# Performance work log

Hardware: AMD Instinct MI355X
Metric: run time of the kernel (lower is better)

## Reference

```python
import jax, jax.numpy as jnp
import numpy as np


def setup_inputs() -> dict:
    key = jax.random.key(0)
    z = jax.random.normal(key, (8, 4096, 1024), dtype=jnp.float32)
    return {"z": z}


def reference(z):
    d = z.shape[-1]
    # sort descending along last dim
    z_sorted = -jnp.sort(-z, axis=-1)
    z_cumsum = jnp.cumsum(z_sorted, axis=-1)
    k = jnp.arange(1, d + 1, dtype=z.dtype)  # [d]
    rhs = 1 + k * z_sorted
    is_gt = (rhs > z_cumsum).astype(z.dtype)
    # largest k satisfying the support condition
    k_z = jnp.max(is_gt * k, axis=-1, keepdims=True)  # [..., 1]
    idx = k_z.astype(jnp.int32) - 1
    z_cumsum_k = jnp.take_along_axis(z_cumsum, idx, axis=-1)
    tau = (z_cumsum_k - 1) / k_z
    p = jnp.clip(z - tau, 0.0, None)
    return p
```

## Files before the change

### kernel.cpp

```cpp
#include <hip/hip_runtime.h>


#define ROW_D 1024

typedef float f4 __attribute__((ext_vector_type(4)));

template <int CTRL, int RMASK>
__device__ __forceinline__ float dpp_mv(float x) {
    return __builtin_bit_cast(float, __builtin_amdgcn_update_dpp(
        __builtin_bit_cast(int, x), __builtin_bit_cast(int, x),
        CTRL, RMASK, 0xf, false));
}

__device__ __forceinline__ float dpp_sum_to63(float x) {
    x += dpp_mv<0x111, 0xf>(x);
    x += dpp_mv<0x112, 0xf>(x);
    x += dpp_mv<0x114, 0xf>(x);
    x += dpp_mv<0x118, 0xf>(x);
    x += dpp_mv<0x142, 0xa>(x);
    x += dpp_mv<0x143, 0xc>(x);
    return x;
}
__device__ __forceinline__ float dpp_max_to63(float x) {
    x = fmaxf(x, dpp_mv<0x111, 0xf>(x));
    x = fmaxf(x, dpp_mv<0x112, 0xf>(x));
    x = fmaxf(x, dpp_mv<0x114, 0xf>(x));
    x = fmaxf(x, dpp_mv<0x118, 0xf>(x));
    x = fmaxf(x, dpp_mv<0x142, 0xa>(x));
    x = fmaxf(x, dpp_mv<0x143, 0xc>(x));
    return x;
}
__device__ __forceinline__ float bcast63(float x) {
    return __builtin_bit_cast(float,
        __builtin_amdgcn_readlane(__builtin_bit_cast(int, x), 63));
}
__device__ __forceinline__ float fast_rcp(float x) {
    float r;
    asm("v_rcp_f32 %0, %1" : "=v"(r) : "v"(x));
    return r;
}

__device__ __forceinline__ void load_row(f4 (&v)[4], const float* __restrict__ z,
                                         int row, int lane) {
    const f4* __restrict__ p = reinterpret_cast<const f4*>(z + (size_t)row * ROW_D);
#pragma unroll
    for (int j = 0; j < 4; ++j) v[j] = p[lane + 64 * j];
}

__device__ __forceinline__ void solve_store(f4 (&v)[4], float* __restrict__ out,
                                            int row, int lane) {
    float mj[4];
#pragma unroll
    for (int j = 0; j < 4; ++j)
        mj[j] = fmaxf(fmaxf(v[j].x, v[j].y), fmaxf(v[j].z, v[j].w));
    float m = fmaxf(fmaxf(mj[0], mj[1]), fmaxf(mj[2], mj[3]));
    m = bcast63(dpp_max_to63(m));

    float t = m - 1.0f;
#pragma unroll 1
    for (int it = 0; it < 16; ++it) {
        float sj[4];
        int n = 0;
#pragma unroll
        for (int j = 0; j < 4; ++j) {
            const float d0 = v[j].x - t, d1 = v[j].y - t;
            const float d2 = v[j].z - t, d3 = v[j].w - t;
            sj[j] = (fmaxf(d0, 0.0f) + fmaxf(d1, 0.0f)) +
                    (fmaxf(d2, 0.0f) + fmaxf(d3, 0.0f));
            n += __popcll(__ballot(d0 > 0.0f));
            n += __popcll(__ballot(d1 > 0.0f));
            n += __popcll(__ballot(d2 > 0.0f));
            n += __popcll(__ballot(d3 > 0.0f));
        }
        const float S = bcast63(dpp_sum_to63((sj[0] + sj[1]) + (sj[2] + sj[3])));
        const float step = (S - 1.0f) * fast_rcp((float)n);
        t += step;
        if (step <= 1e-6f) break;
    }

    f4* __restrict__ p = reinterpret_cast<f4*>(out + (size_t)row * ROW_D);
#pragma unroll
    for (int j = 0; j < 4; ++j) {
        f4 o;
        o.x = fmaxf(v[j].x - t, 0.0f);
        o.y = fmaxf(v[j].y - t, 0.0f);
        o.z = fmaxf(v[j].z - t, 0.0f);
        o.w = fmaxf(v[j].w - t, 0.0f);
        p[lane + 64 * j] = o;
    }
}

__global__ __launch_bounds__(256, 8) void sparsemax_kernel(
    const float* __restrict__ z, float* __restrict__ out, int nrows) {
    const int lane = (int)(threadIdx.x & 63u);
    int r = (int)(blockIdx.x << 2) + (int)(threadIdx.x >> 6);
    const int W = (int)(gridDim.x << 2);
    if (r >= nrows) return;

    f4 A[4], B[4];
    load_row(A, z, r, lane);
    int rn = r + W;
    for (;;) {
        if (rn < nrows) load_row(B, z, rn, lane);
        __builtin_amdgcn_sched_barrier(0);
        solve_store(A, out, r, lane);
        if (rn >= nrows) break;
        r = rn + W;
        if (r < nrows) load_row(A, z, r, lane);
        __builtin_amdgcn_sched_barrier(0);
        solve_store(B, out, rn, lane);
        if (r >= nrows) break;
        rn = r + W;
    }
}

extern "C" void kernel_launch(void* const* d_in, const int* in_sizes, int n_in,
                              void* d_out, int out_size, void* d_ws, size_t ws_size,
                              hipStream_t stream) {
    const float* z = (const float*)d_in[0];
    float* out = (float*)d_out;
    const int n = in_sizes[0];
    const int nrows = n / ROW_D;
    int blocks = 2048;
    const int max_blocks = (nrows + 3) >> 2;
    if (blocks > max_blocks) blocks = max_blocks;
    sparsemax_kernel<<<blocks, 256, 0, stream>>>(z, out, nrows);
}
```

Baseline: 232.2 us.

## Prefetch next row into LDS via global_load_lds and count support with DPP

```diff
diff --git a/kernel.cpp b/kernel.cpp
--- a/kernel.cpp
+++ b/kernel.cpp
@@ -40,15 +40,20 @@
     return r;
 }
 
-__device__ __forceinline__ void load_row(f4 (&v)[4], const float* __restrict__ z,
-                                         int row, int lane) {
-    const f4* __restrict__ p = reinterpret_cast<const f4*>(z + (size_t)row * ROW_D);
+__device__ __forceinline__ void prefetch_row(const float* __restrict__ z,
+                                             int row, int lane,
+                                             float* ldsbase) {
+    const char* g = (const char*)(z + (size_t)row * ROW_D) + (size_t)lane * 16;
 #pragma unroll
-    for (int j = 0; j < 4; ++j) v[j] = p[lane + 64 * j];
+    for (int j = 0; j < 4; ++j) {
+        __builtin_amdgcn_global_load_lds(
+            (const __attribute__((address_space(1))) void*)(g + j * 1024),
+            (__attribute__((address_space(3))) void*)(ldsbase + j * 256),
+            16, 0, 0);
+    }
 }
 
-__device__ __forceinline__ void solve_store(f4 (&v)[4], float* __restrict__ out,
-                                            int row, int lane) {
+__device__ __forceinline__ float solve_tau(const f4 (&v)[4]) {
     float mj[4];
 #pragma unroll
     for (int j = 0; j < 4; ++j)
@@ -59,25 +64,28 @@
     float t = m - 1.0f;
 #pragma unroll 1
     for (int it = 0; it < 16; ++it) {
-        float sj[4];
-        int n = 0;
+        float sj[4], cj[4];
 #pragma unroll
         for (int j = 0; j < 4; ++j) {
             const float d0 = v[j].x - t, d1 = v[j].y - t;
             const float d2 = v[j].z - t, d3 = v[j].w - t;
             sj[j] = (fmaxf(d0, 0.0f) + fmaxf(d1, 0.0f)) +
                     (fmaxf(d2, 0.0f) + fmaxf(d3, 0.0f));
-            n += __popcll(__ballot(d0 > 0.0f));
-            n += __popcll(__ballot(d1 > 0.0f));
-            n += __popcll(__ballot(d2 > 0.0f));
-            n += __popcll(__ballot(d3 > 0.0f));
+            cj[j] = ((d0 > 0.0f ? 1.0f : 0.0f) + (d1 > 0.0f ? 1.0f : 0.0f)) +
+                    ((d2 > 0.0f ? 1.0f : 0.0f) + (d3 > 0.0f ? 1.0f : 0.0f));
         }
         const float S = bcast63(dpp_sum_to63((sj[0] + sj[1]) + (sj[2] + sj[3])));
-        const float step = (S - 1.0f) * fast_rcp((float)n);
+        const float C = bcast63(dpp_sum_to63((cj[0] + cj[1]) + (cj[2] + cj[3])));
+        const float step = (S - 1.0f) * fast_rcp(C);
         t += step;
         if (step <= 1e-6f) break;
     }
+    return t;
+}
 
+__device__ __forceinline__ void store_row(const f4 (&v)[4], float t,
+                                          float* __restrict__ out,
+                                          int row, int lane) {
     f4* __restrict__ p = reinterpret_cast<f4*>(out + (size_t)row * ROW_D);
 #pragma unroll
     for (int j = 0; j < 4; ++j) {
@@ -90,27 +98,41 @@
     }
 }
 
-__global__ __launch_bounds__(256, 8) void sparsemax_kernel(
+__global__ __launch_bounds__(256) void sparsemax_kernel(
     const float* __restrict__ z, float* __restrict__ out, int nrows) {
     const int lane = (int)(threadIdx.x & 63u);
-    int r = (int)(blockIdx.x << 2) + (int)(threadIdx.x >> 6);
+    const int w    = (int)(threadIdx.x >> 6);
+    int r = (int)(blockIdx.x << 2) + w;
     const int W = (int)(gridDim.x << 2);
     if (r >= nrows) return;
 
-    f4 A[4], B[4];
-    load_row(A, z, r, lane);
+    __shared__ float lds[4][2][ROW_D];
+
+    f4 v[4];
+    const f4* __restrict__ zin = reinterpret_cast<const f4*>(z + (size_t)r * ROW_D);
+#pragma unroll
+    for (int j = 0; j < 4; ++j) v[j] = zin[lane + 64 * j];
+
     int rn = r + W;
+    int s = 0;
+    if (rn < nrows) prefetch_row(z, rn, lane, &lds[w][0][0]);
+    __builtin_amdgcn_sched_barrier(0);
+
     for (;;) {
-        if (rn < nrows) load_row(B, z, rn, lane);
+        const float t = solve_tau(v);
+        store_row(v, t, out, r, lane);
+        if (rn >= nrows) break;
+
+        asm volatile("s_waitcnt vmcnt(0)" ::: "memory");
         __builtin_amdgcn_sched_barrier(0);
-        solve_store(A, out, r, lane);
-        if (rn >= nrows) break;
-        r = rn + W;
-        if (r < nrows) load_row(A, z, r, lane);
+        const f4* lsrc = reinterpret_cast<const f4*>(&lds[w][s][0]);
+#pragma unroll
+        for (int j = 0; j < 4; ++j) v[j] = lsrc[lane + 64 * j];
+
+        const int nn = rn + W;
+        if (nn < nrows) prefetch_row(z, nn, lane, &lds[w][s ^ 1][0]);
         __builtin_amdgcn_sched_barrier(0);
-        solve_store(B, out, rn, lane);
-        if (r >= nrows) break;
-        rn = r + W;
+        r = rn; rn = nn; s ^= 1;
     }
 }
 
```

New measurement: 232.8 us. About the same (+0.3%).
